# Optimization experiments

Hardware: AMD Instinct MI355X
Metric: run time of the kernel (lower is better)

Reference implementation:

```python
import jax, jax.numpy as jnp
import numpy as np

SFREQ = 256.0
BANDS = [(0.5, 4.0), (4.0, 8.0), (8.0, 13.0), (13.0, 30.0), (30.0, 50.0)]


def setup_inputs() -> dict:
    key = jax.random.key(0)
    k0, k1, k2 = jax.random.split(key, 3)
    B, T, C, D = 32, 4096, 64, 512
    n_bands = len(BANDS)
    x = jax.random.normal(k0, (B, T, C), dtype=jnp.float32)
    W1 = jax.random.normal(k1, (C * n_bands, D // 2), dtype=jnp.float32) * 0.05
    b1 = jnp.zeros((D // 2,), dtype=jnp.float32)
    W2 = jax.random.normal(k2, (D // 2, D), dtype=jnp.float32) * 0.05
    b2 = jnp.zeros((D,), dtype=jnp.float32)
    return {"x": x, "W1": W1, "b1": b1, "W2": W2, "b2": b2}


def reference(x, W1, b1, W2, b2):
    B, T, C = x.shape
    W = min(int(SFREQ), T)          # window size
    hop = W // 2
    # Static window start indices (overlapping STFT windows)
    starts = np.arange(0, T - W + 1, hop)
    idx = starts[:, None] + np.arange(W)[None, :]            # (nW, W)
    windows = jnp.take(x, jnp.asarray(idx), axis=1)          # (B, nW, W, C)

    # Batched rFFT over the window (time) axis, all windows at once
    xf = jnp.fft.rfft(windows, axis=2)                       # (B, nW, F, C) complex
    power = jnp.abs(xf) ** 2                                  # (B, nW, F, C)

    # Static band masks -> mean over in-band frequency bins (matches masked .mean)
    freqs = np.fft.rfftfreq(W, d=1.0 / SFREQ)
    masks = np.stack([((freqs >= lo) & (freqs <= hi)).astype(np.float32)
                      for lo, hi in BANDS])                   # (5, F)
    masks = masks / masks.sum(axis=1, keepdims=True)
    band = jnp.einsum('bnfc,kf->bnkc', power, jnp.asarray(masks))  # (B, nW, 5, C)
    # torch.cat of per-band (B, C) blocks is band-major -> reshape matches
    feat = band.reshape(B, band.shape[1], -1)                 # (B, nW, 5*C)

    # band_proj MLP
    h = jax.nn.relu(feat @ W1 + b1)
    feat = h @ W2 + b2                                        # (B, nW, D)

    # F.interpolate(mode='linear', align_corners=False) from nW -> T
    nW = feat.shape[1]
    pos = (jnp.arange(T, dtype=jnp.float32) + 0.5) * (nW / T) - 0.5
    pos = jnp.clip(pos, 0.0, float(nW - 1))
    i0 = jnp.floor(pos).astype(jnp.int32)
    i1 = jnp.minimum(i0 + 1, nW - 1)
    w = (pos - i0.astype(jnp.float32))[None, :, None]
    out = feat[:, i0] * (1.0 - w) + feat[:, i1] * w           # (B, T, D)
    return out
```

## Files before the change

### kernel.cpp

```cpp
#include <hip/hip_runtime.h>
#include <hip/hip_bf16.h>
#include <math.h>

#define BB 32
#define TT 4096
#define CC 64
#define DD 512
#define NW 31
#define WIN 256
#define HOP 128
#define NROWS (BB * NW)

typedef float f32x4 __attribute__((ext_vector_type(4)));

__global__ __launch_bounds__(512) void k_bandpower(const float* __restrict__ x,
                                                   float* __restrict__ feat) {
    __shared__ float lds[16384];
    float* u = lds;
    float* v = lds + 8192;

    const int tid = threadIdx.x;
    const int c   = tid & 63;
    const int g   = tid >> 6;
    const int blk = blockIdx.x;
    const int b   = blk / NW;
    const int n   = blk % NW;

    const size_t winBase = ((size_t)b * TT + (size_t)n * HOP) * CC;
    const f32x4* h0 = (const f32x4*)(x + winBase);
    const f32x4* h1 = (const f32x4*)(x + winBase + 128 * CC);
    f32x4* u4 = (f32x4*)u;
    f32x4* v4 = (f32x4*)v;
    for (int i = tid; i < 2048; i += 512) {
        const f32x4 a  = h0[i];
        const f32x4 bb = h1[i];
        u4[i] = a + bb;
        v4[i] = a - bb;
    }
    __syncthreads();

    float coef[7], s1[7], s2[7];
#pragma unroll
    for (int j = 0; j < 7; ++j) {
        const int f = 1 + g + 8 * j;
        coef[j] = 2.0f * cospif((float)f * (1.0f / 128.0f));
        s1[j] = 0.0f;
        s2[j] = 0.0f;
    }
    const float* src = ((g & 1) ? u : v) + c;

#pragma unroll 4
    for (int tt = 0; tt < 128; ++tt) {
        const float xv = src[tt * 64];
#pragma unroll
        for (int j = 0; j < 7; ++j) {
            const float sn = fmaf(coef[j], s1[j], xv - s2[j]);
            s2[j] = s1[j];
            s1[j] = sn;
        }
    }
    __syncthreads();

    float pb[5] = {0.0f, 0.0f, 0.0f, 0.0f, 0.0f};
#pragma unroll
    for (int j = 0; j < 7; ++j) {
        const int f = 1 + g + 8 * j;
        if (f > 50) continue;
        const float p = fmaf(s1[j], s1[j],
                        fmaf(s2[j], s2[j], -coef[j] * s1[j] * s2[j]));
        if (f <= 4)             pb[0] += p;
        if (f >= 4 && f <= 8)   pb[1] += p;
        if (f >= 8 && f <= 13)  pb[2] += p;
        if (f >= 13 && f <= 30) pb[3] += p;
        if (f >= 30)            pb[4] += p;
    }

    float (*bpart)[5][64] = (float (*)[5][64])lds;
#pragma unroll
    for (int k = 0; k < 5; ++k) bpart[g][k][c] = pb[k];
    __syncthreads();

    const float wband[5] = {1.0f / 4.0f, 1.0f / 5.0f, 1.0f / 6.0f,
                            1.0f / 18.0f, 1.0f / 21.0f};
    for (int idx = tid; idx < 320; idx += 512) {
        const int k  = idx >> 6;
        const int cc = idx & 63;
        float s = 0.0f;
#pragma unroll
        for (int gg = 0; gg < 8; ++gg) s += bpart[gg][k][cc];
        feat[(size_t)blk * 320 + idx] = s * wband[k];
    }
}

__global__ __launch_bounds__(256) void k_mlp(const float* __restrict__ feat,
                                             const float* __restrict__ W1,
                                             const float* __restrict__ b1,
                                             const float* __restrict__ W2,
                                             const float* __restrict__ b2,
                                             float* __restrict__ feat2) {
    __shared__ float fs[8][320];
    __shared__ float hs[8][256];

    const int tid  = threadIdx.x;
    const int row0 = blockIdx.x * 8;

    for (int i = tid; i < 8 * 320; i += 256)
        ((float*)fs)[i] = feat[(size_t)row0 * 320 + i];
    __syncthreads();

    float acc[8];
    {
        const float bias = b1[tid];
#pragma unroll
        for (int r = 0; r < 8; ++r) acc[r] = bias;
        for (int i = 0; i < 320; ++i) {
            const float w = W1[(size_t)i * 256 + tid];
#pragma unroll
            for (int r = 0; r < 8; ++r) acc[r] = fmaf(fs[r][i], w, acc[r]);
        }
#pragma unroll
        for (int r = 0; r < 8; ++r) hs[r][tid] = fmaxf(acc[r], 0.0f);
    }
    __syncthreads();

    float o0[8], o1[8];
    {
        const float bias0 = b2[tid];
        const float bias1 = b2[tid + 256];
#pragma unroll
        for (int r = 0; r < 8; ++r) { o0[r] = bias0; o1[r] = bias1; }
        for (int i = 0; i < 256; ++i) {
            const float w0 = W2[(size_t)i * 512 + tid];
            const float w1 = W2[(size_t)i * 512 + tid + 256];
#pragma unroll
            for (int r = 0; r < 8; ++r) {
                const float h = hs[r][i];
                o0[r] = fmaf(h, w0, o0[r]);
                o1[r] = fmaf(h, w1, o1[r]);
            }
        }
    }
#pragma unroll
    for (int r = 0; r < 8; ++r) {
        feat2[(size_t)(row0 + r) * 512 + tid]       = o0[r];
        feat2[(size_t)(row0 + r) * 512 + tid + 256] = o1[r];
    }
}

__global__ __launch_bounds__(256) void k_interp(const float* __restrict__ feat2,
                                                float* __restrict__ out) {
    const int tid  = threadIdx.x;
    const int blk  = blockIdx.x;
    const int b    = blk >> 9;
    const int t0   = (blk & 511) * 8;
    const int d4   = tid & 127;
    const int half = tid >> 7;

#pragma unroll
    for (int it = 0; it < 4; ++it) {
        const int t = t0 + it * 2 + half;
        float pos = ((float)t + 0.5f) * (31.0f / 4096.0f) - 0.5f;
        pos = fminf(fmaxf(pos, 0.0f), 30.0f);
        const int   i0 = (int)pos;
        const int   i1 = min(i0 + 1, 30);
        const float w  = pos - (float)i0;
        const float w0 = 1.0f - w;

        const f32x4* r0 = (const f32x4*)(feat2 + ((size_t)b * NW + i0) * DD);
        const f32x4* r1 = (const f32x4*)(feat2 + ((size_t)b * NW + i1) * DD);
        f32x4* o = (f32x4*)(out + ((size_t)b * TT + t) * DD);
        o[d4] = r0[d4] * w0 + r1[d4] * w;
    }
}

extern "C" void kernel_launch(void* const* d_in, const int* in_sizes, int n_in,
                              void* d_out, int out_size, void* d_ws, size_t ws_size,
                              hipStream_t stream) {
    const float* x  = (const float*)d_in[0];
    const float* W1 = (const float*)d_in[1];
    const float* b1 = (const float*)d_in[2];
    const float* W2 = (const float*)d_in[3];
    const float* b2 = (const float*)d_in[4];
    float* out = (float*)d_out;

    float* feat  = (float*)d_ws;
    float* feat2 = feat + (size_t)NROWS * 320;

    k_bandpower<<<NROWS, 512, 0, stream>>>(x, feat);
    k_mlp<<<NROWS / 8, 256, 0, stream>>>(feat, W1, b1, W2, b2, feat2);
    k_interp<<<16384, 256, 0, stream>>>(feat2, out);
}
```

Baseline: 113.2 us.

## Restructure interpolation by source span to load feature rows once per block

The interpolation kernel now gives each block a half of the time span that maps to one source window index, rather than a fixed group of 8 timesteps. Each thread loads the two neighbouring feature rows once into registers and writes many output rows as va + w*(vb-va). This removes the repeated feature-row loads and per-row index math in the old kernel. The grid shrinks to 1984 blocks with variable work per block (about 66 rows each, edge spans shorter), so the store stream depends on fewer, longer-running blocks. The precision of the blend changes slightly from a*(1-w)+b*w to a+w*(b-a).

```diff
diff --git a/kernel.cpp b/kernel.cpp
--- a/kernel.cpp
+++ b/kernel.cpp
@@ -147,29 +147,50 @@
     }
 }
 
-__global__ __launch_bounds__(256) void k_interp(const float* __restrict__ feat2,
-                                                float* __restrict__ out) {
+__device__ __forceinline__ int i0_of(int t) {
+    float pos = ((float)t + 0.5f) * (31.0f / 4096.0f) - 0.5f;
+    pos = fminf(fmaxf(pos, 0.0f), 30.0f);
+    return (int)pos;
+}
+
+__device__ __forceinline__ int span_start(int i) {
+    if (i <= 0) return 0;
+    if (i >= 31) return TT;
+    int t = (int)(((float)i + 0.5f) * (4096.0f / 31.0f) - 0.5f) - 4;
+    if (t < 0) t = 0;
+    while (t < TT && i0_of(t) < i) ++t;
+    return t;
+}
+
+__global__ __launch_bounds__(256) void k_interp_span(const float* __restrict__ feat2,
+                                                     float* __restrict__ out) {
     const int tid  = threadIdx.x;
     const int blk  = blockIdx.x;
-    const int b    = blk >> 9;
-    const int t0   = (blk & 511) * 8;
+    const int sub  = blk & 1;
+    const int sp   = blk >> 1;
+    const int b    = sp / NW;
+    const int i    = sp % NW;
+    const int r1   = min(i + 1, NW - 1);
     const int d4   = tid & 127;
     const int half = tid >> 7;
 
-#pragma unroll
-    for (int it = 0; it < 4; ++it) {
-        const int t = t0 + it * 2 + half;
+    const f32x4 va = ((const f32x4*)(feat2 + ((size_t)b * NW + i)  * DD))[d4];
+    const f32x4 vb = ((const f32x4*)(feat2 + ((size_t)b * NW + r1) * DD))[d4];
+    const f32x4 vd = vb - va;
+
+    const int tS  = span_start(i);
+    const int tE  = span_start(i + 1);
+    const int mid = tS + ((tE - tS) >> 1);
+    const int t0  = sub ? mid : tS;
+    const int t1  = sub ? tE  : mid;
+
+    for (int t = t0 + half; t < t1; t += 2) {
         float pos = ((float)t + 0.5f) * (31.0f / 4096.0f) - 0.5f;
         pos = fminf(fmaxf(pos, 0.0f), 30.0f);
-        const int   i0 = (int)pos;
-        const int   i1 = min(i0 + 1, 30);
-        const float w  = pos - (float)i0;
-        const float w0 = 1.0f - w;
-
-        const f32x4* r0 = (const f32x4*)(feat2 + ((size_t)b * NW + i0) * DD);
-        const f32x4* r1 = (const f32x4*)(feat2 + ((size_t)b * NW + i1) * DD);
+        const float w = pos - (float)i;
+        const f32x4 res = va + w * vd;
         f32x4* o = (f32x4*)(out + ((size_t)b * TT + t) * DD);
-        o[d4] = r0[d4] * w0 + r1[d4] * w;
+        o[d4] = res;
     }
 }
 
@@ -188,5 +209,5 @@
 
     k_bandpower<<<NROWS, 512, 0, stream>>>(x, feat);
     k_mlp<<<NROWS / 8, 256, 0, stream>>>(feat, W1, b1, W2, b2, feat2);
-    k_interp<<<16384, 256, 0, stream>>>(feat2, out);
-}
+    k_interp_span<<<NROWS * 2, 256, 0, stream>>>(feat2, out);
+}
```

After: 112.8 us. About the same (-0.4%).
